# Kernel tuning notes

Hardware: AMD Instinct MI355X
Metric: run time of the kernel (lower is better)

## Reference

```python
import jax, jax.numpy as jnp
import numpy as np

S = 128      # number of segments
F = 256      # in_features
H = 128      # mlp hidden


def setup_inputs() -> dict:
    key = jax.random.key(0)
    k1, k2, k3 = jax.random.split(key, 3)
    rng = np.random.default_rng(0)
    lengths = rng.integers(1024, 3073, size=S).astype(np.int32)  # ragged segment sizes
    N = int(lengths.sum())  # ~262144 total tokens
    x = jax.random.normal(k1, (N, F), dtype=jnp.float32)
    W1 = jax.random.normal(k2, (F, H), dtype=jnp.float32) * (1.0 / np.sqrt(F))
    b1 = jnp.zeros((H,), dtype=jnp.float32)
    W2 = jax.random.normal(k3, (H, 2), dtype=jnp.float32) * (1.0 / np.sqrt(H))
    b2 = jnp.zeros((2,), dtype=jnp.float32)
    return {"x": x, "lengths": jnp.asarray(lengths), "W1": W1, "b1": b1, "W2": W2, "b2": b2}


def reference(x, lengths, W1, b1, W2, b2):
    N = x.shape[0]
    nseg = lengths.shape[0]
    seg_ids = jnp.repeat(jnp.arange(nseg), lengths, total_repeat_length=N)  # [N]
    offsets = jnp.concatenate([jnp.zeros((1,), lengths.dtype), jnp.cumsum(lengths)[:-1]])
    # position within segment: arange(1, L+1) / L
    pos = (jnp.arange(N) - offsets[seg_ids] + 1).astype(x.dtype)
    Lf = lengths.astype(x.dtype)
    xpos = pos / Lf[seg_ids]  # [N]

    # MLP: Linear -> Tanh -> Linear
    ms = jnp.tanh(x @ W1 + b1) @ W2 + b2  # [N, 2]
    y, z = ms[:, 0], ms[:, 1]

    # per-segment softmax-weighted mean of positions (calc_mean)
    ymax = jax.ops.segment_max(y, seg_ids, num_segments=nseg)
    w = jnp.exp(y - ymax[seg_ids])
    wsum = jax.ops.segment_sum(w, seg_ids, num_segments=nseg)
    means = jax.ops.segment_sum(xpos * w, seg_ids, num_segments=nseg) / wsum  # [S]

    # per-segment softplus(mean(z))
    stds = jax.nn.softplus(jax.ops.segment_sum(z, seg_ids, num_segments=nseg) / Lf)  # [S]

    # normal pdf weights per token
    mu = means[seg_ids]
    sd = stds[seg_ids]
    inv_sqrt_2pi = 1.0 / jnp.sqrt(2.0 * jnp.pi).astype(x.dtype)
    pdf = jnp.exp(-0.5 * ((xpos - mu) / sd) ** 2) * (inv_sqrt_2pi / sd)  # [N]

    # normalize per segment with +0.001 stabilizer
    psum = jax.ops.segment_sum(pdf, seg_ids, num_segments=nseg)
    attn = (pdf / (psum[seg_ids] + 0.001))[:, None]  # [N, 1]

    # attention-weighted sum of features per segment
    out = jax.ops.segment_sum(attn * x, seg_ids, num_segments=nseg)  # [S, F]
    return out, attn
```

## Files before the change

### kernel.cpp

```cpp
#include <hip/hip_runtime.h>
#include <math.h>

#define F 256
#define Hh 128
#define MAXL 3072

typedef short bf16x8 __attribute__((ext_vector_type(8)));
typedef float f32x4 __attribute__((ext_vector_type(4)));
typedef unsigned short ushort4v __attribute__((ext_vector_type(4)));
typedef unsigned short ushort8v __attribute__((ext_vector_type(8)));

__device__ inline unsigned short f2bf_rne(float f) {
  unsigned u = __float_as_uint(f);
  unsigned r = u + 0x7fff + ((u >> 16) & 1);
  return (unsigned short)(r >> 16);
}
__device__ inline float bf2f(unsigned short h) {
  return __uint_as_float((unsigned)h << 16);
}

__global__ void init_kernel(const int* __restrict__ lengths, int* __restrict__ offsets,
                            float* __restrict__ out, const float* __restrict__ W1,
                            unsigned short* __restrict__ whT, unsigned short* __restrict__ wlT,
                            int S, int outN) {
  int t = blockIdx.x * blockDim.x + threadIdx.x;
  int stride = gridDim.x * blockDim.x;
  for (int i = t; i < outN; i += stride) out[i] = 0.f;
  for (int i = t; i < F * Hh; i += stride) {
    int k = i >> 7, col = i & 127;
    float v = W1[i];
    unsigned short h = f2bf_rne(v);
    unsigned short l = f2bf_rne(v - bf2f(h));
    int dst = (k >> 5) * (128 * 32) + col * 32 + (k & 31);
    whT[dst] = h;
    wlT[dst] = l;
  }
  if (blockIdx.x == 0) {
    __shared__ int buf[256];
    int tid = threadIdx.x;
    int v = (tid < S) ? lengths[tid] : 0;
    buf[tid] = v;
    __syncthreads();
    for (int o = 1; o < 256; o <<= 1) {
      int add = (tid >= o) ? buf[tid - o] : 0;
      __syncthreads();
      buf[tid] += add;
      __syncthreads();
    }
    if (tid < S) offsets[tid] = buf[tid] - v;
    if (tid == S - 1) offsets[S] = buf[tid];
  }
}

__global__ __launch_bounds__(256) void mlp_kernel(
    const float* __restrict__ x,
    const unsigned short* __restrict__ whT, const unsigned short* __restrict__ wlT,
    const float* __restrict__ b1, const float* __restrict__ W2,
    const float* __restrict__ b2, float* __restrict__ yv,
    float* __restrict__ zv, int N) {
  __shared__ __align__(16) char SMEM[40960];
  unsigned short* xh = (unsigned short*)SMEM;
  unsigned short* xl = xh + 5120;
  unsigned short* wh = xh + 10240;
  unsigned short* wl = xh + 15360;
  float* red = (float*)SMEM;

  const int t = threadIdx.x;
  const int lane = t & 63;
  const int w = t >> 6;
  const int wr = w >> 1, wc = w & 1;
  const int ln15 = lane & 15, lq = lane >> 4;

  const int row0 = blockIdx.x * 128;

  f32x4 acc[4][4];
#pragma unroll
  for (int i = 0; i < 4; ++i)
#pragma unroll
    for (int j = 0; j < 4; ++j) acc[i][j] = (f32x4){0.f, 0.f, 0.f, 0.f};

  const int xr = t >> 3;
  const int xk = (t & 7) * 4;

  for (int kc = 0; kc < 8; ++kc) {
#pragma unroll
    for (int i = 0; i < 4; ++i) {
      int r = xr + 32 * i;
      int g = row0 + r;
      float4 v = make_float4(0.f, 0.f, 0.f, 0.f);
      if (g < N) v = *(const float4*)&x[(size_t)g * F + kc * 32 + xk];
      ushort4v hv, lv;
      float f[4] = {v.x, v.y, v.z, v.w};
#pragma unroll
      for (int q = 0; q < 4; ++q) {
        unsigned short h = f2bf_rne(f[q]);
        hv[q] = h;
        lv[q] = f2bf_rne(f[q] - bf2f(h));
      }
      *(ushort4v*)&xh[r * 40 + xk] = hv;
      *(ushort4v*)&xl[r * 40 + xk] = lv;
    }
#pragma unroll
    for (int i = 0; i < 2; ++i) {
      int idx = t + 256 * i;
      int col = idx >> 2, k8 = (idx & 3) * 8;
      ushort8v vh = *(const ushort8v*)&whT[kc * 4096 + idx * 8];
      ushort8v vl = *(const ushort8v*)&wlT[kc * 4096 + idx * 8];
      *(ushort8v*)&wh[col * 40 + k8] = vh;
      *(ushort8v*)&wl[col * 40 + k8] = vl;
    }
    __syncthreads();
    bf16x8 bh[4], bl[4];
#pragma unroll
    for (int ct = 0; ct < 4; ++ct) {
      int c = wc * 64 + ct * 16 + ln15;
      bh[ct] = *(const bf16x8*)&wh[c * 40 + lq * 8];
      bl[ct] = *(const bf16x8*)&wl[c * 40 + lq * 8];
    }
#pragma unroll
    for (int rt = 0; rt < 4; ++rt) {
      int r = wr * 64 + rt * 16 + ln15;
      bf16x8 ah = *(const bf16x8*)&xh[r * 40 + lq * 8];
      bf16x8 al = *(const bf16x8*)&xl[r * 40 + lq * 8];
#pragma unroll
      for (int ct = 0; ct < 4; ++ct) {
        acc[rt][ct] = __builtin_amdgcn_mfma_f32_16x16x32_bf16(ah, bh[ct], acc[rt][ct], 0, 0, 0);
        acc[rt][ct] = __builtin_amdgcn_mfma_f32_16x16x32_bf16(ah, bl[ct], acc[rt][ct], 0, 0, 0);
        acc[rt][ct] = __builtin_amdgcn_mfma_f32_16x16x32_bf16(al, bh[ct], acc[rt][ct], 0, 0, 0);
      }
    }
    __syncthreads();
  }

  float yp[4][4], zp[4][4];
#pragma unroll
  for (int i = 0; i < 4; ++i)
#pragma unroll
    for (int j = 0; j < 4; ++j) { yp[i][j] = 0.f; zp[i][j] = 0.f; }
#pragma unroll
  for (int ct = 0; ct < 4; ++ct) {
    int c = wc * 64 + ct * 16 + ln15;
    float b1c = b1[c], wyc = W2[2 * c], wzc = W2[2 * c + 1];
#pragma unroll
    for (int rt = 0; rt < 4; ++rt)
#pragma unroll
      for (int rg = 0; rg < 4; ++rg) {
        float a = acc[rt][ct][rg] + b1c;
        float e = __expf(2.f * a);
        float h = 1.f - __fdividef(2.f, e + 1.f);
        yp[rt][rg] = fmaf(h, wyc, yp[rt][rg]);
        zp[rt][rg] = fmaf(h, wzc, zp[rt][rg]);
      }
  }
#pragma unroll
  for (int rt = 0; rt < 4; ++rt)
#pragma unroll
    for (int rg = 0; rg < 4; ++rg)
      red[(wr * 64 + rt * 16 + lq * 4 + rg) * 33 + wc * 16 + ln15] = yp[rt][rg];
  __syncthreads();
  if (t < 128) {
    float s = 0.f;
#pragma unroll
    for (int q = 0; q < 32; ++q) s += red[t * 33 + q];
    int g = row0 + t;
    if (g < N) yv[g] = s + b2[0];
  }
  __syncthreads();
#pragma unroll
  for (int rt = 0; rt < 4; ++rt)
#pragma unroll
    for (int rg = 0; rg < 4; ++rg)
      red[(wr * 64 + rt * 16 + lq * 4 + rg) * 33 + wc * 16 + ln15] = zp[rt][rg];
  __syncthreads();
  if (t < 128) {
    float s = 0.f;
#pragma unroll
    for (int q = 0; q < 32; ++q) s += red[t * 33 + q];
    int g = row0 + t;
    if (g < N) zv[g] = s + b2[1];
  }
}

__device__ inline float wave_reduce_sum(float v) {
#pragma unroll
  for (int o = 32; o; o >>= 1) v += __shfl_down(v, o);
  return v;
}
__device__ inline float wave_reduce_max(float v) {
#pragma unroll
  for (int o = 32; o; o >>= 1) v = fmaxf(v, __shfl_down(v, o));
  return v;
}

__global__ __launch_bounds__(256) void stats_kernel(
    const float* __restrict__ yv, const float* __restrict__ zv,
    const int* __restrict__ offsets, const int* __restrict__ lengths,
    float* __restrict__ attn) {
  __shared__ float ybuf[MAXL];
  __shared__ float zbuf[MAXL];
  __shared__ float redA[4], redB[4], redC[4];
  const int s = blockIdx.x;
  const int off = offsets[s];
  const int L = lengths[s];
  const int t = threadIdx.x;
  const int lane = t & 63, wid = t >> 6;

  float lmax = -1e30f;
  for (int i = t; i < L; i += 256) {
    float yy = yv[off + i];
    ybuf[i] = yy;
    zbuf[i] = zv[off + i];
    lmax = fmaxf(lmax, yy);
  }
  lmax = wave_reduce_max(lmax);
  if (lane == 0) redA[wid] = lmax;
  __syncthreads();
  const float ymax = fmaxf(fmaxf(redA[0], redA[1]), fmaxf(redA[2], redA[3]));
  const float invL = 1.f / (float)L;
  __syncthreads();

  float sw = 0.f, smx = 0.f, sz = 0.f;
  for (int i = t; i < L; i += 256) {
    float wgt = __expf(ybuf[i] - ymax);
    float xp = (float)(i + 1) * invL;
    sw += wgt;
    smx = fmaf(xp, wgt, smx);
    sz += zbuf[i];
  }
  sw = wave_reduce_sum(sw);
  smx = wave_reduce_sum(smx);
  sz = wave_reduce_sum(sz);
  if (lane == 0) { redA[wid] = sw; redB[wid] = smx; redC[wid] = sz; }
  __syncthreads();
  const float wsum = redA[0] + redA[1] + redA[2] + redA[3];
  const float mxs  = redB[0] + redB[1] + redB[2] + redB[3];
  const float zsum = redC[0] + redC[1] + redC[2] + redC[3];
  const float mu = mxs / wsum;
  const float tz = zsum * invL;
  const float sd = fmaxf(tz, 0.f) + log1pf(__expf(-fabsf(tz)));
  const float invsd = 1.f / sd;
  const float C = 0.3989422804014327f;
  __syncthreads();

  float ps = 0.f;
  for (int i = t; i < L; i += 256) {
    float xp = (float)(i + 1) * invL;
    float u = (xp - mu) * invsd;
    float p = __expf(-0.5f * u * u) * (C * invsd);
    ybuf[i] = p;
    ps += p;
  }
  ps = wave_reduce_sum(ps);
  if (lane == 0) redA[wid] = ps;
  __syncthreads();
  const float psum = redA[0] + redA[1] + redA[2] + redA[3];
  const float sc = 1.f / (psum + 0.001f);
  for (int i = t; i < L; i += 256) attn[off + i] = ybuf[i] * sc;
}

__global__ __launch_bounds__(256) void pool_kernel(
    const float* __restrict__ x, const float* __restrict__ attn,
    const int* __restrict__ offsets, const int* __restrict__ lengths,
    float* __restrict__ out, int nchunks) {
  const int s = blockIdx.x, c = blockIdx.y;
  const int off = offsets[s], L = lengths[s];
  const int i0 = (int)((long long)L * c / nchunks);
  const int i1 = (int)((long long)L * (c + 1) / nchunks);
  const int f = threadIdx.x;
  float acc[4] = {0.f, 0.f, 0.f, 0.f};
  int i = i0;
  for (; i + 3 < i1; i += 4) {
#pragma unroll
    for (int q = 0; q < 4; ++q)
      acc[q] = fmaf(attn[off + i + q], x[(size_t)(off + i + q) * F + f], acc[q]);
  }
  for (; i < i1; ++i)
    acc[0] = fmaf(attn[off + i], x[(size_t)(off + i) * F + f], acc[0]);
  float a = (acc[0] + acc[1]) + (acc[2] + acc[3]);
  atomicAdd(&out[s * F + f], a);
}

extern "C" void kernel_launch(void* const* d_in, const int* in_sizes, int n_in,
                              void* d_out, int out_size, void* d_ws, size_t ws_size,
                              hipStream_t stream) {
  const float* x      = (const float*)d_in[0];
  const int* lengths  = (const int*)d_in[1];
  const float* W1     = (const float*)d_in[2];
  const float* b1     = (const float*)d_in[3];
  const float* W2     = (const float*)d_in[4];
  const float* b2     = (const float*)d_in[5];
  const int S = in_sizes[1];
  const int N = in_sizes[0] / F;

  float* out  = (float*)d_out;
  float* attn = out + (size_t)S * F;

  int*   offsets = (int*)d_ws;
  float* yv = (float*)d_ws + 512;
  float* zv = yv + N;
  unsigned short* whT = (unsigned short*)(zv + N);
  unsigned short* wlT = whT + F * Hh;

  init_kernel<<<64, 256, 0, stream>>>(lengths, offsets, out, W1, whT, wlT, S, S * F);
  mlp_kernel<<<(N + 127) / 128, 256, 0, stream>>>(x, whT, wlT, b1, W2, b2, yv, zv, N);
  stats_kernel<<<S, 256, 0, stream>>>(yv, zv, offsets, lengths, attn);
  pool_kernel<<<dim3(S, 32), 256, 0, stream>>>(x, attn, offsets, lengths, out, 32);
}
```

Baseline: 512.7 us.

## Load MLP operands directly into registers, widen stats blocks, vectorize pooling

The MLP kernel now loads x rows and the bf16 weight fragments straight from global memory into MFMA registers instead of staging them through shared memory. This drops the LDS round trip and both per-chunk barriers, and the output reduction now uses wave shuffles. The stats kernel moves to 1024-thread blocks, and the pooling kernel has each wave read float4 rows, then combines the partial sums in LDS before issuing the atomics. The MLP change gives up coalescing: each lane makes strided row loads and re-reads the weights from global memory without block-level reuse.

```diff
diff --git a/kernel.cpp b/kernel.cpp
--- a/kernel.cpp
+++ b/kernel.cpp
@@ -7,8 +7,6 @@
 
 typedef short bf16x8 __attribute__((ext_vector_type(8)));
 typedef float f32x4 __attribute__((ext_vector_type(4)));
-typedef unsigned short ushort4v __attribute__((ext_vector_type(4)));
-typedef unsigned short ushort8v __attribute__((ext_vector_type(8)));
 
 __device__ inline unsigned short f2bf_rne(float f) {
   unsigned u = __float_as_uint(f);
@@ -58,12 +56,8 @@
     const float* __restrict__ b1, const float* __restrict__ W2,
     const float* __restrict__ b2, float* __restrict__ yv,
     float* __restrict__ zv, int N) {
-  __shared__ __align__(16) char SMEM[40960];
-  unsigned short* xh = (unsigned short*)SMEM;
-  unsigned short* xl = xh + 5120;
-  unsigned short* wh = xh + 10240;
-  unsigned short* wl = xh + 15360;
-  float* red = (float*)SMEM;
+  __shared__ float redy[128][2];
+  __shared__ float redz[128][2];
 
   const int t = threadIdx.x;
   const int lane = t & 63;
@@ -79,49 +73,45 @@
 #pragma unroll
     for (int j = 0; j < 4; ++j) acc[i][j] = (f32x4){0.f, 0.f, 0.f, 0.f};
 
-  const int xr = t >> 3;
-  const int xk = (t & 7) * 4;
+  int rowg[4];
+  bool rv[4];
+#pragma unroll
+  for (int rt = 0; rt < 4; ++rt) {
+    rowg[rt] = row0 + wr * 64 + rt * 16 + ln15;
+    rv[rt] = rowg[rt] < N;
+  }
+  const int cbase = wc * 64 + ln15;
 
   for (int kc = 0; kc < 8; ++kc) {
-#pragma unroll
-    for (int i = 0; i < 4; ++i) {
-      int r = xr + 32 * i;
-      int g = row0 + r;
-      float4 v = make_float4(0.f, 0.f, 0.f, 0.f);
-      if (g < N) v = *(const float4*)&x[(size_t)g * F + kc * 32 + xk];
-      ushort4v hv, lv;
-      float f[4] = {v.x, v.y, v.z, v.w};
-#pragma unroll
-      for (int q = 0; q < 4; ++q) {
+    float4 av0[4], av1[4];
+#pragma unroll
+    for (int rt = 0; rt < 4; ++rt) {
+      av0[rt] = make_float4(0.f, 0.f, 0.f, 0.f);
+      av1[rt] = make_float4(0.f, 0.f, 0.f, 0.f);
+      if (rv[rt]) {
+        const float* p = &x[(size_t)rowg[rt] * F + kc * 32 + lq * 8];
+        av0[rt] = *(const float4*)p;
+        av1[rt] = *(const float4*)(p + 4);
+      }
+    }
+    bf16x8 bh[4], bl[4];
+#pragma unroll
+    for (int ct = 0; ct < 4; ++ct) {
+      int o = kc * 4096 + (cbase + ct * 16) * 32 + lq * 8;
+      bh[ct] = *(const bf16x8*)&whT[o];
+      bl[ct] = *(const bf16x8*)&wlT[o];
+    }
+#pragma unroll
+    for (int rt = 0; rt < 4; ++rt) {
+      float f[8] = {av0[rt].x, av0[rt].y, av0[rt].z, av0[rt].w,
+                    av1[rt].x, av1[rt].y, av1[rt].z, av1[rt].w};
+      bf16x8 ah, al;
+#pragma unroll
+      for (int q = 0; q < 8; ++q) {
         unsigned short h = f2bf_rne(f[q]);
-        hv[q] = h;
-        lv[q] = f2bf_rne(f[q] - bf2f(h));
-      }
-      *(ushort4v*)&xh[r * 40 + xk] = hv;
-      *(ushort4v*)&xl[r * 40 + xk] = lv;
-    }
-#pragma unroll
-    for (int i = 0; i < 2; ++i) {
-      int idx = t + 256 * i;
-      int col = idx >> 2, k8 = (idx & 3) * 8;
-      ushort8v vh = *(const ushort8v*)&whT[kc * 4096 + idx * 8];
-      ushort8v vl = *(const ushort8v*)&wlT[kc * 4096 + idx * 8];
-      *(ushort8v*)&wh[col * 40 + k8] = vh;
-      *(ushort8v*)&wl[col * 40 + k8] = vl;
-    }
-    __syncthreads();
-    bf16x8 bh[4], bl[4];
-#pragma unroll
-    for (int ct = 0; ct < 4; ++ct) {
-      int c = wc * 64 + ct * 16 + ln15;
-      bh[ct] = *(const bf16x8*)&wh[c * 40 + lq * 8];
-      bl[ct] = *(const bf16x8*)&wl[c * 40 + lq * 8];
-    }
-#pragma unroll
-    for (int rt = 0; rt < 4; ++rt) {
-      int r = wr * 64 + rt * 16 + ln15;
-      bf16x8 ah = *(const bf16x8*)&xh[r * 40 + lq * 8];
-      bf16x8 al = *(const bf16x8*)&xl[r * 40 + lq * 8];
+        ah[q] = (short)h;
+        al[q] = (short)f2bf_rne(f[q] - bf2f(h));
+      }
 #pragma unroll
       for (int ct = 0; ct < 4; ++ct) {
         acc[rt][ct] = __builtin_amdgcn_mfma_f32_16x16x32_bf16(ah, bh[ct], acc[rt][ct], 0, 0, 0);
@@ -129,7 +119,6 @@
         acc[rt][ct] = __builtin_amdgcn_mfma_f32_16x16x32_bf16(al, bh[ct], acc[rt][ct], 0, 0, 0);
       }
     }
-    __syncthreads();
   }
 
   float yp[4][4], zp[4][4];
@@ -139,7 +128,7 @@
     for (int j = 0; j < 4; ++j) { yp[i][j] = 0.f; zp[i][j] = 0.f; }
 #pragma unroll
   for (int ct = 0; ct < 4; ++ct) {
-    int c = wc * 64 + ct * 16 + ln15;
+    int c = cbase + ct * 16;
     float b1c = b1[c], wyc = W2[2 * c], wzc = W2[2 * c + 1];
 #pragma unroll
     for (int rt = 0; rt < 4; ++rt)
@@ -155,29 +144,26 @@
 #pragma unroll
   for (int rt = 0; rt < 4; ++rt)
 #pragma unroll
-    for (int rg = 0; rg < 4; ++rg)
-      red[(wr * 64 + rt * 16 + lq * 4 + rg) * 33 + wc * 16 + ln15] = yp[rt][rg];
+    for (int rg = 0; rg < 4; ++rg) {
+      float vy = yp[rt][rg], vz = zp[rt][rg];
+#pragma unroll
+      for (int m = 8; m; m >>= 1) {
+        vy += __shfl_xor(vy, m);
+        vz += __shfl_xor(vz, m);
+      }
+      if (ln15 == 0) {
+        int row = wr * 64 + rt * 16 + lq * 4 + rg;
+        redy[row][wc] = vy;
+        redz[row][wc] = vz;
+      }
+    }
   __syncthreads();
   if (t < 128) {
-    float s = 0.f;
-#pragma unroll
-    for (int q = 0; q < 32; ++q) s += red[t * 33 + q];
     int g = row0 + t;
-    if (g < N) yv[g] = s + b2[0];
-  }
-  __syncthreads();
-#pragma unroll
-  for (int rt = 0; rt < 4; ++rt)
-#pragma unroll
-    for (int rg = 0; rg < 4; ++rg)
-      red[(wr * 64 + rt * 16 + lq * 4 + rg) * 33 + wc * 16 + ln15] = zp[rt][rg];
-  __syncthreads();
-  if (t < 128) {
-    float s = 0.f;
-#pragma unroll
-    for (int q = 0; q < 32; ++q) s += red[t * 33 + q];
-    int g = row0 + t;
-    if (g < N) zv[g] = s + b2[1];
+    if (g < N) {
+      yv[g] = redy[t][0] + redy[t][1] + b2[0];
+      zv[g] = redz[t][0] + redz[t][1] + b2[1];
+    }
   }
 }
 
@@ -192,13 +178,13 @@
   return v;
 }
 
-__global__ __launch_bounds__(256) void stats_kernel(
+__global__ __launch_bounds__(1024) void stats_kernel(
     const float* __restrict__ yv, const float* __restrict__ zv,
     const int* __restrict__ offsets, const int* __restrict__ lengths,
     float* __restrict__ attn) {
   __shared__ float ybuf[MAXL];
   __shared__ float zbuf[MAXL];
-  __shared__ float redA[4], redB[4], redC[4];
+  __shared__ float redA[16], redB[16], redC[16];
   const int s = blockIdx.x;
   const int off = offsets[s];
   const int L = lengths[s];
@@ -206,7 +192,7 @@
   const int lane = t & 63, wid = t >> 6;
 
   float lmax = -1e30f;
-  for (int i = t; i < L; i += 256) {
+  for (int i = t; i < L; i += 1024) {
     float yy = yv[off + i];
     ybuf[i] = yy;
     zbuf[i] = zv[off + i];
@@ -215,12 +201,14 @@
   lmax = wave_reduce_max(lmax);
   if (lane == 0) redA[wid] = lmax;
   __syncthreads();
-  const float ymax = fmaxf(fmaxf(redA[0], redA[1]), fmaxf(redA[2], redA[3]));
+  float ymax = redA[0];
+#pragma unroll
+  for (int q = 1; q < 16; ++q) ymax = fmaxf(ymax, redA[q]);
   const float invL = 1.f / (float)L;
   __syncthreads();
 
   float sw = 0.f, smx = 0.f, sz = 0.f;
-  for (int i = t; i < L; i += 256) {
+  for (int i = t; i < L; i += 1024) {
     float wgt = __expf(ybuf[i] - ymax);
     float xp = (float)(i + 1) * invL;
     sw += wgt;
@@ -232,9 +220,9 @@
   sz = wave_reduce_sum(sz);
   if (lane == 0) { redA[wid] = sw; redB[wid] = smx; redC[wid] = sz; }
   __syncthreads();
-  const float wsum = redA[0] + redA[1] + redA[2] + redA[3];
-  const float mxs  = redB[0] + redB[1] + redB[2] + redB[3];
-  const float zsum = redC[0] + redC[1] + redC[2] + redC[3];
+  float wsum = 0.f, mxs = 0.f, zsum = 0.f;
+#pragma unroll
+  for (int q = 0; q < 16; ++q) { wsum += redA[q]; mxs += redB[q]; zsum += redC[q]; }
   const float mu = mxs / wsum;
   const float tz = zsum * invL;
   const float sd = fmaxf(tz, 0.f) + log1pf(__expf(-fabsf(tz)));
@@ -243,7 +231,7 @@
   __syncthreads();
 
   float ps = 0.f;
-  for (int i = t; i < L; i += 256) {
+  for (int i = t; i < L; i += 1024) {
     float xp = (float)(i + 1) * invL;
     float u = (xp - mu) * invsd;
     float p = __expf(-0.5f * u * u) * (C * invsd);
@@ -253,31 +241,60 @@
   ps = wave_reduce_sum(ps);
   if (lane == 0) redA[wid] = ps;
   __syncthreads();
-  const float psum = redA[0] + redA[1] + redA[2] + redA[3];
+  float psum = 0.f;
+#pragma unroll
+  for (int q = 0; q < 16; ++q) psum += redA[q];
   const float sc = 1.f / (psum + 0.001f);
-  for (int i = t; i < L; i += 256) attn[off + i] = ybuf[i] * sc;
+  for (int i = t; i < L; i += 1024) attn[off + i] = ybuf[i] * sc;
 }
 
 __global__ __launch_bounds__(256) void pool_kernel(
     const float* __restrict__ x, const float* __restrict__ attn,
     const int* __restrict__ offsets, const int* __restrict__ lengths,
     float* __restrict__ out, int nchunks) {
+  __shared__ float4 sbuf[4][64];
   const int s = blockIdx.x, c = blockIdx.y;
   const int off = offsets[s], L = lengths[s];
   const int i0 = (int)((long long)L * c / nchunks);
   const int i1 = (int)((long long)L * (c + 1) / nchunks);
-  const int f = threadIdx.x;
-  float acc[4] = {0.f, 0.f, 0.f, 0.f};
-  int i = i0;
-  for (; i + 3 < i1; i += 4) {
-#pragma unroll
-    for (int q = 0; q < 4; ++q)
-      acc[q] = fmaf(attn[off + i + q], x[(size_t)(off + i + q) * F + f], acc[q]);
-  }
-  for (; i < i1; ++i)
-    acc[0] = fmaf(attn[off + i], x[(size_t)(off + i) * F + f], acc[0]);
-  float a = (acc[0] + acc[1]) + (acc[2] + acc[3]);
-  atomicAdd(&out[s * F + f], a);
+  const int t = threadIdx.x;
+  const int lane = t & 63, wid = t >> 6;
+
+  float4 a0 = make_float4(0.f, 0.f, 0.f, 0.f);
+  float4 a1 = make_float4(0.f, 0.f, 0.f, 0.f);
+  int i = i0 + wid;
+  for (; i + 4 < i1; i += 8) {
+    float w0 = attn[off + i];
+    float w1 = attn[off + i + 4];
+    float4 v0 = *(const float4*)&x[(size_t)(off + i) * F + lane * 4];
+    float4 v1 = *(const float4*)&x[(size_t)(off + i + 4) * F + lane * 4];
+    a0.x = fmaf(w0, v0.x, a0.x); a0.y = fmaf(w0, v0.y, a0.y);
+    a0.z = fmaf(w0, v0.z, a0.z); a0.w = fmaf(w0, v0.w, a0.w);
+    a1.x = fmaf(w1, v1.x, a1.x); a1.y = fmaf(w1, v1.y, a1.y);
+    a1.z = fmaf(w1, v1.z, a1.z); a1.w = fmaf(w1, v1.w, a1.w);
+  }
+  if (i < i1) {
+    float w0 = attn[off + i];
+    float4 v0 = *(const float4*)&x[(size_t)(off + i) * F + lane * 4];
+    a0.x = fmaf(w0, v0.x, a0.x); a0.y = fmaf(w0, v0.y, a0.y);
+    a0.z = fmaf(w0, v0.z, a0.z); a0.w = fmaf(w0, v0.w, a0.w);
+  }
+  a0.x += a1.x; a0.y += a1.y; a0.z += a1.z; a0.w += a1.w;
+  sbuf[wid][lane] = a0;
+  __syncthreads();
+  if (wid == 0) {
+    float4 r0 = sbuf[0][lane], r1 = sbuf[1][lane];
+    float4 r2 = sbuf[2][lane], r3 = sbuf[3][lane];
+    float rx = (r0.x + r1.x) + (r2.x + r3.x);
+    float ry = (r0.y + r1.y) + (r2.y + r3.y);
+    float rz = (r0.z + r1.z) + (r2.z + r3.z);
+    float rw = (r0.w + r1.w) + (r2.w + r3.w);
+    float* o = &out[s * F + lane * 4];
+    atomicAdd(o + 0, rx);
+    atomicAdd(o + 1, ry);
+    atomicAdd(o + 2, rz);
+    atomicAdd(o + 3, rw);
+  }
 }
 
 extern "C" void kernel_launch(void* const* d_in, const int* in_sizes, int n_in,
@@ -303,6 +320,6 @@
 
   init_kernel<<<64, 256, 0, stream>>>(lengths, offsets, out, W1, whT, wlT, S, S * F);
   mlp_kernel<<<(N + 127) / 128, 256, 0, stream>>>(x, whT, wlT, b1, W2, b2, yv, zv, N);
-  stats_kernel<<<S, 256, 0, stream>>>(yv, zv, offsets, lengths, attn);
+  stats_kernel<<<S, 1024, 0, stream>>>(yv, zv, offsets, lengths, attn);
   pool_kernel<<<dim3(S, 32), 256, 0, stream>>>(x, attn, offsets, lengths, out, 32);
 }
```

Result: faster. 462.5 us (-9.8%).
